# Kernel tuning notes

Hardware: AMD Instinct MI355X
Metric: run time of the kernel (lower is better)

## Reference

```python
import jax, jax.numpy as jnp
import numpy as np

EPS = 1e-8  # matches torch F.cosine_similarity default eps


def _flatten_spatial(x):
    # [B, C, d, h, w] -> [B, N, C]
    B, C = x.shape[:2]
    return x.reshape(B, C, -1).transpose(0, 2, 1)


def _stage_loss(canon_src, canon_tgt, src_desc, tgt_desc):
    stage_size = src_desc.shape[2:]
    B, C = canon_src.shape[:2]
    # trilinear resize with half-pixel centers == torch align_corners=False
    rs = jax.image.resize(canon_src, (B, C) + stage_size, method='trilinear')
    rt = jax.image.resize(canon_tgt, (B, C) + stage_size, method='trilinear')
    a = _flatten_spatial(rs)  # [B, N, 3]
    b = _flatten_spatial(rt)  # [B, N, 3]
    # squared euclidean distances (argmin is invariant to sqrt)
    a2 = jnp.sum(a * a, axis=-1)  # [B, N]
    b2 = jnp.sum(b * b, axis=-1)  # [B, N]
    ab = jnp.einsum('bnc,bmc->bnm', a, b)  # [B, N, N]
    d2 = a2[:, :, None] + b2[:, None, :] - 2.0 * ab
    nearest = jnp.argmin(d2, axis=-1)  # [B, N] int
    sd = _flatten_spatial(src_desc)  # [B, N, Cd]
    td = _flatten_spatial(tgt_desc)  # [B, N, Cd]
    gathered = jnp.take_along_axis(td, nearest[:, :, None], axis=1)  # [B, N, Cd]
    num = jnp.sum(sd * gathered, axis=-1)
    denom = jnp.maximum(jnp.linalg.norm(sd, axis=-1), EPS) * \
            jnp.maximum(jnp.linalg.norm(gathered, axis=-1), EPS)
    cos = num / denom
    return 1.0 - jnp.mean(cos)


def setup_inputs() -> dict:
    key = jax.random.key(0)
    ks = jax.random.split(key, 6)
    return {
        'canonical_source': jax.random.normal(ks[0], (4, 3, 64, 64, 64), jnp.float32),
        'canonical_target': jax.random.normal(ks[1], (4, 3, 64, 64, 64), jnp.float32),
        'src_desc0': jax.random.normal(ks[2], (4, 32, 16, 16, 16), jnp.float32),
        'tgt_desc0': jax.random.normal(ks[3], (4, 32, 16, 16, 16), jnp.float32),
        'src_desc1': jax.random.normal(ks[4], (4, 32, 8, 8, 8), jnp.float32),
        'tgt_desc1': jax.random.normal(ks[5], (4, 32, 8, 8, 8), jnp.float32),
    }


def reference(canonical_source, canonical_target, src_desc0, tgt_desc0, src_desc1, tgt_desc1):
    l0 = _stage_loss(canonical_source, canonical_target, src_desc0, tgt_desc0)
    l1 = _stage_loss(canonical_source, canonical_target, src_desc1, tgt_desc1)
    return jnp.stack([l0, l1]).mean()
```

## Files before the change

### kernel.cpp

```cpp
#include <hip/hip_runtime.h>
#include <cfloat>

typedef unsigned long long u64;

#define CDESC 32
#define N0 4096
#define N1 512

__device__ __forceinline__ unsigned fbits_mono(float d) {
    unsigned b = __float_as_uint(d);
    return (d >= 0.f) ? (b | 0x80000000u) : ~b;
}

__device__ __forceinline__ void wave_reduce_atomic(float v, float* acc) {
#pragma unroll
    for (int off = 32; off > 0; off >>= 1) v += __shfl_down(v, off, 64);
    if ((threadIdx.x & 63) == 0) atomicAdd(acc, v);
}

__global__ __launch_bounds__(256) void pass1_fused(
        const float* __restrict__ csrc, const float* __restrict__ ctgt,
        const float* __restrict__ sd0, const float* __restrict__ td0,
        const float* __restrict__ sd1, const float* __restrict__ td1,
        float* __restrict__ x16a, float* __restrict__ x16b,
        float* __restrict__ x8a,  float* __restrict__ x8b,
        float* __restrict__ sd0T, float* __restrict__ td0T,
        float* __restrict__ sd1T, float* __restrict__ td1T,
        float* __restrict__ acc) {
    __shared__ __align__(16) float sRow[65 * 64];
    __shared__ float xf16[64 * 17];
    __shared__ float xf8[64 * 9];
    const int tid = threadIdx.x;
    const int bx  = blockIdx.x, by = blockIdx.y;
    if (by == 0 && bx == 0 && tid < 4) acc[tid] = 0.f;

    if (bx < 768) {
        int bc = bx >> 6, z = bx & 63;
        const float* in = by ? ctgt : csrc;
        float* o16 = by ? x16b : x16a;
        float* o8  = by ? x8b  : x8a;
        const float4* src = (const float4*)(in + (size_t)(bc * 64 + z) * 4096);
#pragma unroll
        for (int k = 0; k < 4; ++k) {
            float4 v = src[tid + k * 256];
            int g = tid + k * 256;
            int y = g >> 4, j = (g & 15) * 4;
            float* p = &sRow[y * 65 + j];
            p[0] = v.x; p[1] = v.y; p[2] = v.z; p[3] = v.w;
        }
        __syncthreads();
#pragma unroll
        for (int k = 0; k < 6; ++k) {
            int o = tid + k * 256;
            if (o < 1024) {
                int y = o >> 4, xo = o & 15;
                int j0 = 4 * xo - 2;
                float sum = 0.f, wsum = 0.f;
#pragma unroll
                for (int t = 0; t < 8; ++t) {
                    int j = j0 + t;
                    float w = 1.f - fabsf((float)t - 3.5f) / 4.f;
                    if (j >= 0 && j < 64) { sum = fmaf(w, sRow[y * 65 + j], sum); wsum += w; }
                }
                xf16[y * 17 + xo] = sum / wsum;
            } else {
                int o2 = o - 1024;
                int y = o2 >> 3, xo = o2 & 7;
                int j0 = 8 * xo - 4;
                float sum = 0.f, wsum = 0.f;
#pragma unroll
                for (int t = 0; t < 16; ++t) {
                    int j = j0 + t;
                    float w = 1.f - fabsf((float)t - 7.5f) / 8.f;
                    if (j >= 0 && j < 64) { sum = fmaf(w, sRow[y * 65 + j], sum); wsum += w; }
                }
                xf8[y * 9 + xo] = sum / wsum;
            }
        }
        __syncthreads();
        {
            int y2 = tid >> 4, x = tid & 15;
            int j0 = 4 * y2 - 2;
            float sum = 0.f, wsum = 0.f;
#pragma unroll
            for (int t = 0; t < 8; ++t) {
                int j = j0 + t;
                float w = 1.f - fabsf((float)t - 3.5f) / 4.f;
                if (j >= 0 && j < 64) { sum = fmaf(w, xf16[j * 17 + x], sum); wsum += w; }
            }
            o16[bc * 16384 + z * 256 + y2 * 16 + x] = sum / wsum;
        }
        if (tid < 64) {
            int y2 = tid >> 3, x = tid & 7;
            int j0 = 8 * y2 - 4;
            float sum = 0.f, wsum = 0.f;
#pragma unroll
            for (int t = 0; t < 16; ++t) {
                int j = j0 + t;
                float w = 1.f - fabsf((float)t - 7.5f) / 8.f;
                if (j >= 0 && j < 64) { sum = fmaf(w, xf8[j * 9 + x], sum); wsum += w; }
            }
            o8[bc * 4096 + z * 64 + y2 * 8 + x] = sum / wsum;
        }
    } else {
        __shared__ float tile[64 * 33];
        int tl = bx - 768;
        const float* din; float* dout; int N, b, n0;
        if (tl < 256) { din = by ? td0 : sd0; dout = by ? td0T : sd0T;
                        N = N0; b = tl >> 6; n0 = (tl & 63) * 64; }
        else { tl -= 256; din = by ? td1 : sd1; dout = by ? td1T : sd1T;
               N = N1; b = tl >> 3; n0 = (tl & 7) * 64; }
#pragma unroll
        for (int i = 0; i < 8; ++i) {
            int idx = tid + i * 256;
            int c = idx >> 6, j = idx & 63;
            tile[j * 33 + c] = din[((size_t)b * CDESC + c) * N + n0 + j];
        }
        __syncthreads();
#pragma unroll
        for (int i = 0; i < 8; ++i) {
            int idx = tid + i * 256;
            int p = idx >> 5, c = idx & 31;
            dout[((size_t)b * N + n0 + p) * CDESC + c] = tile[p * 33 + c];
        }
    }
}

__global__ __launch_bounds__(256) void pass2z(
        const float* __restrict__ x16a, const float* __restrict__ x16b,
        const float* __restrict__ x8a,  const float* __restrict__ x8b,
        float4* __restrict__ ps0, float4* __restrict__ pt0,
        float4* __restrict__ ps1, float4* __restrict__ pt1) {
    int gid = blockIdx.x * 256 + threadIdx.x;
    if (blockIdx.x < 128) {
        int side = gid >> 14, r = gid & 16383;
        int b = r >> 12, n = r & 4095;
        int x = n & 15, y = (n >> 4) & 15, z = n >> 8;
        const float* t = side ? x16b : x16a;
        const float* base = t + (size_t)b * 49152 + y * 16 + x;
        float a0 = 0.f, a1 = 0.f, a2 = 0.f, wzs = 0.f;
#pragma unroll
        for (int tt = 0; tt < 8; ++tt) {
            float w = 1.f - fabsf((float)tt - 3.5f) * 0.25f;
            int jz = 4 * z - 2 + tt;
            if ((unsigned)jz < 64u) {
                const float* p = base + jz * 256;
                a0 = fmaf(w, p[0],     a0);
                a1 = fmaf(w, p[16384], a1);
                a2 = fmaf(w, p[32768], a2);
                wzs += w;
            }
        }
        float inv = 1.f / wzs;
        a0 *= inv; a1 *= inv; a2 *= inv;
        float sq = a0 * a0 + a1 * a1 + a2 * a2;
        if (side) pt0[b * N0 + n] = make_float4(-2.f * a0, -2.f * a1, -2.f * a2, sq);
        else      ps0[b * N0 + n] = make_float4(a0, a1, a2, sq);
    } else {
        int g = gid - 32768;
        int side = g >> 11, r = g & 2047;
        int b = r >> 9, n = r & 511;
        int x = n & 7, y = (n >> 3) & 7, z = n >> 6;
        const float* t = side ? x8b : x8a;
        const float* base = t + (size_t)b * 12288 + y * 8 + x;
        float a0 = 0.f, a1 = 0.f, a2 = 0.f, wzs = 0.f;
#pragma unroll
        for (int tt = 0; tt < 16; ++tt) {
            float w = 1.f - fabsf((float)tt - 7.5f) * 0.125f;
            int jz = 8 * z - 4 + tt;
            if ((unsigned)jz < 64u) {
                const float* p = base + jz * 64;
                a0 = fmaf(w, p[0],    a0);
                a1 = fmaf(w, p[4096], a1);
                a2 = fmaf(w, p[8192], a2);
                wzs += w;
            }
        }
        float inv = 1.f / wzs;
        a0 *= inv; a1 *= inv; a2 *= inv;
        float sq = a0 * a0 + a1 * a1 + a2 * a2;
        if (side) pt1[b * N1 + n] = make_float4(-2.f * a0, -2.f * a1, -2.f * a2, sq);
        else      ps1[b * N1 + n] = make_float4(a0, a1, a2, sq);
    }
}

__device__ __forceinline__ float cos_pm(const float* __restrict__ sT,
                                        const float* __restrict__ tT,
                                        size_t si, size_t ti) {
    const float4* s = (const float4*)(sT + si * CDESC);
    const float4* t = (const float4*)(tT + ti * CDESC);
    float num = 0.f, s2 = 0.f, t2 = 0.f;
#pragma unroll
    for (int c = 0; c < 8; ++c) {
        float4 a = s[c], g = t[c];
        num = fmaf(a.x, g.x, fmaf(a.y, g.y, fmaf(a.z, g.z, fmaf(a.w, g.w, num))));
        s2  = fmaf(a.x, a.x, fmaf(a.y, a.y, fmaf(a.z, a.z, fmaf(a.w, a.w, s2))));
        t2  = fmaf(g.x, g.x, fmaf(g.y, g.y, fmaf(g.z, g.z, fmaf(g.w, g.w, t2))));
    }
    return num / (fmaxf(sqrtf(s2), 1e-8f) * fmaxf(sqrtf(t2), 1e-8f));
}

__device__ __forceinline__ float dist_pm(float4 P, float4 Q) {
    return fmaf(P.x, Q.x, fmaf(P.y, Q.y, fmaf(P.z, Q.z, Q.w)));
}

__global__ __launch_bounds__(256) void nn_cos_all(
        const float4* __restrict__ ps0, const float4* __restrict__ pt0,
        const float* __restrict__ sd0T, const float* __restrict__ td0T,
        const float4* __restrict__ ps1, const float4* __restrict__ pt1,
        const float* __restrict__ sd1T, const float* __restrict__ td1T,
        float* acc, float* __restrict__ out) {
    extern __shared__ __align__(16) char smraw[];
    float4* sm = (float4*)smraw;
    const int tid = threadIdx.x;
    const int bx  = blockIdx.x;

    if (bx < 256) {
        int b = bx >> 6, ptile = bx & 63;
        const float4* tp = pt0 + b * N0;
        for (int i = tid; i < N0; i += 256)
            sm[i] = tp[i];
        __syncthreads();
        int w = tid >> 6, lane = tid & 63;
        int n = ptile * 64 + lane;
        float4 P = ps0[b * N0 + n];
        const int m0 = w * 1024;
        float best = FLT_MAX; int bbase = 0;
        for (int k0 = 0; k0 < 1024; k0 += 16) {
            float d[16];
#pragma unroll
            for (int u = 0; u < 16; ++u)
                d[u] = dist_pm(P, sm[m0 + k0 + u]);
            float e0 = fminf(d[0],  d[1]),  e1 = fminf(d[2],  d[3]);
            float e2 = fminf(d[4],  d[5]),  e3 = fminf(d[6],  d[7]);
            float e4 = fminf(d[8],  d[9]),  e5 = fminf(d[10], d[11]);
            float e6 = fminf(d[12], d[13]), e7 = fminf(d[14], d[15]);
            float f0 = fminf(e0, e1), f1 = fminf(e2, e3);
            float f2 = fminf(e4, e5), f3 = fminf(e6, e7);
            float bm = fminf(fminf(f0, f1), fminf(f2, f3));
            if (bm < best) { best = bm; bbase = k0; }
        }
        int bi = 0;
#pragma unroll
        for (int u = 15; u >= 0; --u) {
            float dv = dist_pm(P, sm[m0 + bbase + u]);
            if (dv == best) bi = u;
        }
        u64 key = ((u64)fbits_mono(best) << 32) | (unsigned)(m0 + bbase + bi);
        __syncthreads();
        u64* keys = (u64*)smraw;
        keys[w * 64 + lane] = key;
        __syncthreads();
        if (tid < 64) {
            u64 k0 = keys[tid],       k1 = keys[tid + 64];
            u64 k2 = keys[tid + 128], k3 = keys[tid + 192];
            u64 ka = k0 < k1 ? k0 : k1;
            u64 kb = k2 < k3 ? k2 : k3;
            u64 kk = ka < kb ? ka : kb;
            int nearest = (int)(unsigned)(kk & 0xFFFFFFFFull);
            int n2 = ptile * 64 + tid;
            float cosv = cos_pm(sd0T, td0T, (size_t)b * N0 + n2,
                                (size_t)b * N0 + nearest);
            wave_reduce_atomic(cosv, acc + 0);
        }
    } else {
        int bb = bx - 256;
        int b = bb >> 1;
        const float4* tp = pt1 + b * N1;
        for (int i = tid; i < N1; i += 256)
            sm[i] = tp[i];
        __syncthreads();
        int n = (bb & 1) * 256 + tid;
        float4 P = ps1[b * N1 + n];
        float best = FLT_MAX; int bbase = 0;
        for (int k0 = 0; k0 < N1; k0 += 16) {
            float d[16];
#pragma unroll
            for (int u = 0; u < 16; ++u)
                d[u] = dist_pm(P, sm[k0 + u]);
            float e0 = fminf(d[0],  d[1]),  e1 = fminf(d[2],  d[3]);
            float e2 = fminf(d[4],  d[5]),  e3 = fminf(d[6],  d[7]);
            float e4 = fminf(d[8],  d[9]),  e5 = fminf(d[10], d[11]);
            float e6 = fminf(d[12], d[13]), e7 = fminf(d[14], d[15]);
            float f0 = fminf(e0, e1), f1 = fminf(e2, e3);
            float f2 = fminf(e4, e5), f3 = fminf(e6, e7);
            float bm = fminf(fminf(f0, f1), fminf(f2, f3));
            if (bm < best) { best = bm; bbase = k0; }
        }
        int bi = 0;
#pragma unroll
        for (int u = 15; u >= 0; --u) {
            float dv = dist_pm(P, sm[bbase + u]);
            if (dv == best) bi = u;
        }
        float cosv = cos_pm(sd1T, td1T, (size_t)b * N1 + n,
                            (size_t)b * N1 + bbase + bi);
        wave_reduce_atomic(cosv, acc + 1);
    }

    __syncthreads();
    if (tid == 0) {
        __threadfence();
        unsigned old = atomicAdd((unsigned*)(acc + 2), 1u);
        if (old == 263u) {
            float a0 = atomicAdd(acc + 0, 0.f);
            float a1 = atomicAdd(acc + 1, 0.f);
            out[0] = 1.f - 0.5f * (a0 * (1.f / 16384.f) + a1 * (1.f / 2048.f));
        }
    }
}

extern "C" void kernel_launch(void* const* d_in, const int* in_sizes, int n_in,
                              void* d_out, int out_size, void* d_ws, size_t ws_size,
                              hipStream_t stream) {
    const float* c_src = (const float*)d_in[0];
    const float* c_tgt = (const float*)d_in[1];
    const float* sd0   = (const float*)d_in[2];
    const float* td0   = (const float*)d_in[3];
    const float* sd1   = (const float*)d_in[4];
    const float* td1   = (const float*)d_in[5];
    float* out = (float*)d_out;

    char* ws = (char*)d_ws;
    float* acc  = (float*)ws;
    float* x16a = (float*)(ws + 256);
    float* x16b = x16a + 196608;
    float* x8a  = x16b + 196608;
    float* x8b  = x8a + 49152;
    float4* ps0 = (float4*)(x8b + 49152);
    float4* pt0 = ps0 + 16384;
    float4* ps1 = pt0 + 16384;
    float4* pt1 = ps1 + 2048;
    float* sd0T = (float*)(pt1 + 2048);
    float* td0T = sd0T + 524288;
    float* sd1T = td0T + 524288;
    float* td1T = sd1T + 65536;

    pass1_fused<<<dim3(1056, 2), 256, 0, stream>>>(c_src, c_tgt, sd0, td0, sd1, td1,
                                                   x16a, x16b, x8a, x8b,
                                                   sd0T, td0T, sd1T, td1T, acc);
    pass2z<<<144, 256, 0, stream>>>(x16a, x16b, x8a, x8b, ps0, pt0, ps1, pt1);
    nn_cos_all<<<264, 256, 65536, stream>>>(ps0, pt0, sd0T, td0T, ps1, pt1,
                                            sd1T, td1T, acc, out);
}
```

Baseline: 116.5 us.

## Broadcast target points via readlane instead of staging them in shared memory

The nearest-neighbour kernel stops copying the whole target point set into 64KB of LDS. Each lane now loads one float4 target from global memory per 64-point chunk and broadcasts it to the whole wave with readlane. This removes the LDS fill, a block barrier, and the LDS reads in the inner loop, and it frees LDS for occupancy. The cost is four readlane scalar moves per target point, which may limit issue rate, plus global reads in the final rescan to recover the index.

New measurement: 123.9 us. 1.06x slower.

```diff
diff --git a/kernel.cpp b/kernel.cpp
--- a/kernel.cpp
+++ b/kernel.cpp
@@ -16,6 +16,10 @@
 #pragma unroll
     for (int off = 32; off > 0; off >>= 1) v += __shfl_down(v, off, 64);
     if ((threadIdx.x & 63) == 0) atomicAdd(acc, v);
+}
+
+__device__ __forceinline__ float bcast(float v, int L) {
+    return __int_as_float(__builtin_amdgcn_readlane(__float_as_int(v), L));
 }
 
 __global__ __launch_bounds__(256) void pass1_fused(
@@ -204,51 +208,63 @@
     return fmaf(P.x, Q.x, fmaf(P.y, Q.y, fmaf(P.z, Q.z, Q.w)));
 }
 
+#define DIST16(darr, Qv, G)                                                    \
+    _Pragma("unroll")                                                          \
+    for (int u = 0; u < 16; ++u) {                                             \
+        float qx = bcast((Qv).x, (G) * 16 + u);                                \
+        float qy = bcast((Qv).y, (G) * 16 + u);                                \
+        float qz = bcast((Qv).z, (G) * 16 + u);                                \
+        float qw = bcast((Qv).w, (G) * 16 + u);                                \
+        darr[u] = fmaf(P.x, qx, fmaf(P.y, qy, fmaf(P.z, qz, qw)));             \
+    }
+
+#define MINTREE16(darr, bm)                                                    \
+    float e0 = fminf(darr[0],  darr[1]),  e1 = fminf(darr[2],  darr[3]);       \
+    float e2 = fminf(darr[4],  darr[5]),  e3 = fminf(darr[6],  darr[7]);       \
+    float e4 = fminf(darr[8],  darr[9]),  e5 = fminf(darr[10], darr[11]);      \
+    float e6 = fminf(darr[12], darr[13]), e7 = fminf(darr[14], darr[15]);      \
+    float f0 = fminf(e0, e1), f1 = fminf(e2, e3);                              \
+    float f2 = fminf(e4, e5), f3 = fminf(e6, e7);                              \
+    float bm = fminf(fminf(f0, f1), fminf(f2, f3));
+
 __global__ __launch_bounds__(256) void nn_cos_all(
         const float4* __restrict__ ps0, const float4* __restrict__ pt0,
         const float* __restrict__ sd0T, const float* __restrict__ td0T,
         const float4* __restrict__ ps1, const float4* __restrict__ pt1,
         const float* __restrict__ sd1T, const float* __restrict__ td1T,
         float* acc, float* __restrict__ out) {
-    extern __shared__ __align__(16) char smraw[];
-    float4* sm = (float4*)smraw;
+    __shared__ u64 keys[256];
     const int tid = threadIdx.x;
     const int bx  = blockIdx.x;
+    const int lane = tid & 63;
 
     if (bx < 256) {
         int b = bx >> 6, ptile = bx & 63;
-        const float4* tp = pt0 + b * N0;
-        for (int i = tid; i < N0; i += 256)
-            sm[i] = tp[i];
-        __syncthreads();
-        int w = tid >> 6, lane = tid & 63;
+        int w = tid >> 6;
         int n = ptile * 64 + lane;
         float4 P = ps0[b * N0 + n];
-        const int m0 = w * 1024;
+        const float4* tp = pt0 + b * N0 + w * 1024;
         float best = FLT_MAX; int bbase = 0;
-        for (int k0 = 0; k0 < 1024; k0 += 16) {
-            float d[16];
-#pragma unroll
-            for (int u = 0; u < 16; ++u)
-                d[u] = dist_pm(P, sm[m0 + k0 + u]);
-            float e0 = fminf(d[0],  d[1]),  e1 = fminf(d[2],  d[3]);
-            float e2 = fminf(d[4],  d[5]),  e3 = fminf(d[6],  d[7]);
-            float e4 = fminf(d[8],  d[9]),  e5 = fminf(d[10], d[11]);
-            float e6 = fminf(d[12], d[13]), e7 = fminf(d[14], d[15]);
-            float f0 = fminf(e0, e1), f1 = fminf(e2, e3);
-            float f2 = fminf(e4, e5), f3 = fminf(e6, e7);
-            float bm = fminf(fminf(f0, f1), fminf(f2, f3));
-            if (bm < best) { best = bm; bbase = k0; }
+        for (int k0 = 0; k0 < 1024; k0 += 64) {
+            float4 Q4 = tp[k0 + lane];
+#pragma unroll
+            for (int g = 0; g < 4; ++g) {
+                float d[16];
+                DIST16(d, Q4, g)
+                MINTREE16(d, bm)
+                if (bm < best) { best = bm; bbase = k0 + g * 16; }
+            }
         }
         int bi = 0;
-#pragma unroll
-        for (int u = 15; u >= 0; --u) {
-            float dv = dist_pm(P, sm[m0 + bbase + u]);
-            if (dv == best) bi = u;
-        }
-        u64 key = ((u64)fbits_mono(best) << 32) | (unsigned)(m0 + bbase + bi);
-        __syncthreads();
-        u64* keys = (u64*)smraw;
+        {
+            const float4* tpr = tp + bbase;
+#pragma unroll
+            for (int u = 15; u >= 0; --u) {
+                float dv = dist_pm(P, tpr[u]);
+                if (dv == best) bi = u;
+            }
+        }
+        u64 key = ((u64)fbits_mono(best) << 32) | (unsigned)(w * 1024 + bbase + bi);
         keys[w * 64 + lane] = key;
         __syncthreads();
         if (tid < 64) {
@@ -266,32 +282,28 @@
     } else {
         int bb = bx - 256;
         int b = bb >> 1;
-        const float4* tp = pt1 + b * N1;
-        for (int i = tid; i < N1; i += 256)
-            sm[i] = tp[i];
-        __syncthreads();
         int n = (bb & 1) * 256 + tid;
         float4 P = ps1[b * N1 + n];
+        const float4* tp = pt1 + b * N1;
         float best = FLT_MAX; int bbase = 0;
-        for (int k0 = 0; k0 < N1; k0 += 16) {
-            float d[16];
-#pragma unroll
-            for (int u = 0; u < 16; ++u)
-                d[u] = dist_pm(P, sm[k0 + u]);
-            float e0 = fminf(d[0],  d[1]),  e1 = fminf(d[2],  d[3]);
-            float e2 = fminf(d[4],  d[5]),  e3 = fminf(d[6],  d[7]);
-            float e4 = fminf(d[8],  d[9]),  e5 = fminf(d[10], d[11]);
-            float e6 = fminf(d[12], d[13]), e7 = fminf(d[14], d[15]);
-            float f0 = fminf(e0, e1), f1 = fminf(e2, e3);
-            float f2 = fminf(e4, e5), f3 = fminf(e6, e7);
-            float bm = fminf(fminf(f0, f1), fminf(f2, f3));
-            if (bm < best) { best = bm; bbase = k0; }
+        for (int k0 = 0; k0 < N1; k0 += 64) {
+            float4 Q4 = tp[k0 + lane];
+#pragma unroll
+            for (int g = 0; g < 4; ++g) {
+                float d[16];
+                DIST16(d, Q4, g)
+                MINTREE16(d, bm)
+                if (bm < best) { best = bm; bbase = k0 + g * 16; }
+            }
         }
         int bi = 0;
-#pragma unroll
-        for (int u = 15; u >= 0; --u) {
-            float dv = dist_pm(P, sm[bbase + u]);
-            if (dv == best) bi = u;
+        {
+            const float4* tpr = tp + bbase;
+#pragma unroll
+            for (int u = 15; u >= 0; --u) {
+                float dv = dist_pm(P, tpr[u]);
+                if (dv == best) bi = u;
+            }
         }
         float cosv = cos_pm(sd1T, td1T, (size_t)b * N1 + n,
                             (size_t)b * N1 + bbase + bi);
@@ -340,6 +352,6 @@
                                                    x16a, x16b, x8a, x8b,
                                                    sd0T, td0T, sd1T, td1T, acc);
     pass2z<<<144, 256, 0, stream>>>(x16a, x16b, x8a, x8b, ps0, pt0, ps1, pt1);
-    nn_cos_all<<<264, 256, 65536, stream>>>(ps0, pt0, sd0T, td0T, ps1, pt1,
-                                            sd1T, td1T, acc, out);
-}
+    nn_cos_all<<<264, 256, 0, stream>>>(ps0, pt0, sd0T, td0T, ps1, pt1,
+                                        sd1T, td1T, acc, out);
+}
```
